# Kernel optimization log

Hardware: AMD Instinct MI355X
Metric: run time of the kernel (lower is better)

## Reference

```python
import jax, jax.numpy as jnp
import numpy as np

INPUT_DIM = 128
HIDDEN_DIM = 128
N_PATIENTS = 200000
N_CONDITIONS = 5000
N_EDGES = 1000000
IN_FEAT = INPUT_DIM * 2 + 1  # 257


def _linear_params(key, fan_in, fan_out):
    # torch nn.Linear default init: U(-1/sqrt(fan_in), 1/sqrt(fan_in))
    kw, kb = jax.random.split(key)
    bound = 1.0 / np.sqrt(fan_in)
    W = jax.random.uniform(kw, (fan_in, fan_out), jnp.float32, -bound, bound)
    b = jax.random.uniform(kb, (fan_out,), jnp.float32, -bound, bound)
    return W, b


def setup_inputs() -> dict:
    key = jax.random.key(0)
    ks = jax.random.split(key, 8)
    patient_embeds = jax.random.normal(ks[0], (N_PATIENTS, INPUT_DIM), jnp.float32)
    condition_embeds = jax.random.normal(ks[1], (N_CONDITIONS, INPUT_DIM), jnp.float32)
    src_idx = jax.random.randint(ks[2], (N_EDGES,), 0, N_PATIENTS)
    dst_idx = jax.random.randint(ks[3], (N_EDGES,), 0, N_CONDITIONS)
    edge_index = jnp.stack([src_idx, dst_idx], axis=0)
    tte = jax.random.uniform(ks[4], (N_EDGES,), jnp.float32)
    W1, b1 = _linear_params(ks[5], IN_FEAT, HIDDEN_DIM)
    W2, b2 = _linear_params(ks[6], HIDDEN_DIM, HIDDEN_DIM)
    k7, k8 = jax.random.split(ks[7])
    Wo, bo = _linear_params(k7, HIDDEN_DIM, 1)
    Wr, br = _linear_params(k8, IN_FEAT, HIDDEN_DIM)
    return {
        "patient_embeds": patient_embeds,
        "condition_embeds": condition_embeds,
        "edge_index": edge_index,
        "tte": tte,
        "W1": W1, "b1": b1,
        "W2": W2, "b2": b2,
        "Wo": Wo, "bo": bo,
        "Wr": Wr, "br": br,
    }


def reference(patient_embeds, condition_embeds, edge_index, tte,
              W1, b1, W2, b2, Wo, bo, Wr, br):
    src = patient_embeds[edge_index[0]]        # [E, D]
    dst = condition_embeds[edge_index[1]]      # [E, D]
    x = jnp.concatenate([src, dst, tte[:, None]], axis=1)  # [E, 2D+1]
    h1 = jax.nn.relu(x @ W1 + b1)              # [E, H]
    res = x @ Wr + br                          # [E, H]
    h2 = jax.nn.relu(h1 @ W2 + b2 + res)       # [E, H]
    return (h2 @ Wo + bo).reshape(-1)          # [E]
```

## Files before the change

kernel.cpp:

```cpp
#include <hip/hip_runtime.h>
#include <hip/hip_bf16.h>

using u16   = unsigned short;
using u16x4 = __attribute__((ext_vector_type(4))) unsigned short;
using u16x8 = __attribute__((ext_vector_type(8))) unsigned short;
using s16x8 = __attribute__((ext_vector_type(8))) short;
using f32x4 = __attribute__((ext_vector_type(4))) float;

#define KPAD 136
#define XP   136
#define OP   264
#define EB   64

#define BARRIER() asm volatile("s_waitcnt lgkmcnt(0)\n\ts_barrier" ::: "memory")

__device__ __forceinline__ float bf2f(u16 u){
  unsigned int x = ((unsigned int)u) << 16;
  float f; __builtin_memcpy(&f, &x, 4); return f;
}
__device__ __forceinline__ u16 f2bf(float f){
  __hip_bfloat16 h = __float2bfloat16(f);
  u16 u; __builtin_memcpy(&u, &h, 2); return u;
}
__device__ __forceinline__ f32x4 mfma16(s16x8 a, s16x8 b, f32x4 c){
  return __builtin_amdgcn_mfma_f32_16x16x32_bf16(a, b, c, 0, 0, 0);
}

__global__ __launch_bounds__(256) void prep_kernel(
    const float* __restrict__ W1, const float* __restrict__ W2,
    const float* __restrict__ Wo, const float* __restrict__ Wr,
    const float* __restrict__ b1, const float* __restrict__ b2,
    const float* __restrict__ br,
    u16* __restrict__ WF, u16* __restrict__ W2T, float* __restrict__ params)
{
  const int tid = blockIdx.x*256 + threadIdx.x;
  const int nth = gridDim.x*256;
  for (int id = tid; id < 131072; id += nth){
    const int j    = id & 7;
    const int lane = (id >> 3) & 63;
    const int pair = (id >> 9) & 1;
    const int ks   = (id >> 10) & 3;
    const int nb   = (id >> 12) & 15;
    const int h    = (id >> 16) & 1;
    const int k = ks*32 + (lane >> 4)*8 + j;
    const int n = nb*16 + (lane & 15);
    const float v = ((n < 128) ? W1 : Wr)[(h*128 + k)*128 + (n & 127)];
    const u16 hi = f2bf(v);
    WF[id] = pair ? f2bf(v - bf2f(hi)) : hi;
  }
  for (int id = tid; id < 128*128; id += nth){
    const int k = id >> 7, n = id & 127;
    W2T[n*KPAD + k] = f2bf(W2[k*128 + n]);
  }
  for (int id = tid; id < 128; id += nth){
    params[id]       = W1[256*128 + id];
    params[128 + id] = Wr[256*128 + id];
    params[256 + id] = Wo[id];
    params[384 + id]       = b1[id];
    params[384 + 128 + id] = br[id] + b2[id];
  }
}

__global__ __launch_bounds__(512, 4) void mm_kernel(
    const float* __restrict__ emb, int nrows, int ntiles,
    const u16* __restrict__ WFh, const float* __restrict__ bias,
    u16* __restrict__ outbuf)
{
  __shared__ __align__(16) char smem_raw[64*XP*2*2];
  u16* xhi = (u16*)smem_raw;
  u16* xlo = xhi + 64*XP;
  u16* sO  = (u16*)smem_raw;
  const int t = threadIdx.x;
  const int l = t & 63, w = t >> 6;
  const int lrow = l & 15, lq = l >> 4;
  s16x8 wf[2][4][2];
#pragma unroll
  for (int nbh = 0; nbh < 2; ++nbh)
#pragma unroll
    for (int ks = 0; ks < 4; ++ks){
      const int nb = w + nbh*8;
      const u16* base = WFh + (size_t)((nb*4 + ks)*2)*512 + l*8;
      wf[nbh][ks][0] = *(const s16x8*)(base);
      wf[nbh][ks][1] = *(const s16x8*)(base + 512);
    }
  float bv[2][4] = {{0.f,0.f,0.f,0.f},{0.f,0.f,0.f,0.f}};
  if (bias){
#pragma unroll
    for (int nbh = 0; nbh < 2; ++nbh)
#pragma unroll
      for (int r = 0; r < 4; ++r)
        bv[nbh][r] = bias[(w + nbh*8)*16 + lq*4 + r];
  }
  for (int tile = blockIdx.x; tile < ntiles; tile += gridDim.x){
    const int row0 = tile*64;
    BARRIER();
#pragma unroll
    for (int i = 0; i < 4; ++i){
      const int f4 = i*512 + t;
      const int r = f4 >> 5, kc = f4 & 31;
      int grow = row0 + r; if (grow >= nrows) grow = nrows - 1;
      const float4 v = *(const float4*)(emb + (size_t)grow*128 + kc*4);
      const float vv[4] = {v.x, v.y, v.z, v.w};
      u16x4 h4, l4;
#pragma unroll
      for (int q = 0; q < 4; ++q){
        const u16 hi = f2bf(vv[q]);
        h4[q] = hi;
        l4[q] = f2bf(vv[q] - bf2f(hi));
      }
      *(u16x4*)(xhi + r*XP + kc*4) = h4;
      *(u16x4*)(xlo + r*XP + kc*4) = l4;
    }
    BARRIER();
    f32x4 acc[2][4];
#pragma unroll
    for (int a = 0; a < 2; ++a)
#pragma unroll
      for (int b = 0; b < 4; ++b) acc[a][b] = (f32x4){0.f,0.f,0.f,0.f};
#pragma unroll
    for (int mb = 0; mb < 4; ++mb){
      const int mro = (mb*16 + lrow)*XP + lq*8;
#pragma unroll
      for (int ks = 0; ks < 4; ++ks){
        const s16x8 xh = *(const s16x8*)(xhi + mro + ks*32);
        const s16x8 xl = *(const s16x8*)(xlo + mro + ks*32);
#pragma unroll
        for (int nbh = 0; nbh < 2; ++nbh){
          acc[nbh][mb] = mfma16(wf[nbh][ks][0], xh, acc[nbh][mb]);
          acc[nbh][mb] = mfma16(wf[nbh][ks][1], xh, acc[nbh][mb]);
          acc[nbh][mb] = mfma16(wf[nbh][ks][0], xl, acc[nbh][mb]);
        }
      }
    }
    BARRIER();
#pragma unroll
    for (int nbh = 0; nbh < 2; ++nbh)
#pragma unroll
      for (int mb = 0; mb < 4; ++mb){
        const int m = mb*16 + lrow;
        u16x4 o;
#pragma unroll
        for (int r = 0; r < 4; ++r) o[r] = f2bf(acc[nbh][mb][r] + bv[nbh][r]);
        *(u16x4*)(sO + m*OP + (w + nbh*8)*16 + lq*4) = o;
      }
    BARRIER();
#pragma unroll
    for (int i = 0; i < 4; ++i){
      const int idx = i*512 + t;
      const int m = idx >> 5, c = idx & 31;
      const int grow = row0 + m;
      if (grow < nrows){
        const u16x8 v = *(const u16x8*)(sO + m*OP + c*8);
        *(u16x8*)(outbuf + (size_t)grow*256 + c*8) = v;
      }
    }
  }
}

__global__ __launch_bounds__(512, 4) void edge_kernel(
    const int* __restrict__ ei, const float* __restrict__ tte,
    const u16* __restrict__ PP, const u16* __restrict__ CC,
    const u16* __restrict__ W2T, const float* __restrict__ params,
    const float* __restrict__ bo_p, float* __restrict__ out, int E, int ntiles)
{
  __shared__ u16 sW2T[128*KPAD];
  __shared__ u16 sA[EB*KPAD];
  __shared__ u16 sR[EB*KPAD];
  __shared__ float sw1t[128], swrt[128], sWo[128];
  __shared__ float souts[4][EB];
  const int t = threadIdx.x;
  const int l = t & 63, w = t >> 6;
  const int lrow = l & 15, lk = l >> 4;
  const int rh = w & 1, ch = w >> 1;
  const int gid = t >> 5, gl = t & 31;
  const float bo = bo_p[0];
  {
    const u16x8* g = (const u16x8*)W2T;
    u16x8* s = (u16x8*)sW2T;
    for (int i = t; i < 128*KPAD/8; i += 512) s[i] = g[i];
  }
  if (t < 128){ sw1t[t] = params[t]; swrt[t] = params[128+t]; sWo[t] = params[256+t]; }

  int tile = blockIdx.x;
  if (tile >= ntiles) return;
  float ctt[4];
  u16x8 cpv[4], ccv[4];
  {
    int cs[4], cd[4];
#pragma unroll
    for (int i = 0; i < 4; ++i){
      int e = tile*EB + i*16 + gid; if (e >= E) e = E - 1;
      cs[i] = ei[e]; cd[i] = ei[E + e]; ctt[i] = tte[e];
    }
#pragma unroll
    for (int i = 0; i < 4; ++i){
      cpv[i] = *(const u16x8*)(PP + (size_t)cs[i]*256 + gl*8);
      ccv[i] = *(const u16x8*)(CC + (size_t)cd[i]*256 + gl*8);
    }
  }
  BARRIER();

  for (; tile < ntiles; tile += gridDim.x){
    const int ntile = tile + gridDim.x;
#pragma unroll
    for (int i = 0; i < 4; ++i){
      const int e = i*16 + gid;
      const int jj = (gl & 15)*8;
      const float tt = ctt[i];
      const float* wt = (gl < 16) ? (sw1t + jj) : (swrt + jj);
      u16x8 o;
#pragma unroll
      for (int q = 0; q < 8; ++q){
        float v = bf2f(cpv[i][q]) + bf2f(ccv[i][q]) + tt * wt[q];
        if (gl < 16) v = fmaxf(v, 0.f);
        o[q] = f2bf(v);
      }
      u16* dst = (gl < 16) ? (sA + e*KPAD + jj) : (sR + e*KPAD + jj);
      *(u16x8*)dst = o;
    }
    u16x8 npv[4], ncv[4];
    float ntt[4];
    {
      int nxs[4], nxd[4];
#pragma unroll
      for (int i = 0; i < 4; ++i){
        int e = ntile*EB + i*16 + gid; if (e >= E) e = E - 1;
        nxs[i] = ei[e]; nxd[i] = ei[E + e]; ntt[i] = tte[e];
      }
#pragma unroll
      for (int i = 0; i < 4; ++i){
        npv[i] = *(const u16x8*)(PP + (size_t)nxs[i]*256 + gl*8);
        ncv[i] = *(const u16x8*)(CC + (size_t)nxd[i]*256 + gl*8);
      }
    }
    BARRIER();
    f32x4 acc[2][2];
#pragma unroll
    for (int a = 0; a < 2; ++a)
#pragma unroll
      for (int b = 0; b < 2; ++b) acc[a][b] = (f32x4){0.f,0.f,0.f,0.f};
#pragma unroll
    for (int ks = 0; ks < 4; ++ks){
      const int koff = ks*32 + lk*8;
      const s16x8 h0 = *(const s16x8*)(sA + (rh*32 + lrow)*KPAD + koff);
      const s16x8 h1 = *(const s16x8*)(sA + (rh*32 + 16 + lrow)*KPAD + koff);
      const s16x8 b0 = *(const s16x8*)(sW2T + (ch*32 + lrow)*KPAD + koff);
      const s16x8 b1 = *(const s16x8*)(sW2T + (ch*32 + 16 + lrow)*KPAD + koff);
      acc[0][0] = mfma16(b0, h0, acc[0][0]);
      acc[0][1] = mfma16(b0, h1, acc[0][1]);
      acc[1][0] = mfma16(b1, h0, acc[1][0]);
      acc[1][1] = mfma16(b1, h1, acc[1][1]);
    }
    float p[2] = {0.f, 0.f};
    float wo[2][4];
#pragma unroll
    for (int nb = 0; nb < 2; ++nb){
#pragma unroll
      for (int r = 0; r < 4; ++r) wo[nb][r] = sWo[ch*32 + nb*16 + lk*4 + r];
    }
#pragma unroll
    for (int mb = 0; mb < 2; ++mb){
      const int edge = rh*32 + mb*16 + lrow;
#pragma unroll
      for (int nb = 0; nb < 2; ++nb){
        const int col0 = ch*32 + nb*16 + lk*4;
        const u16x4 rv = *(const u16x4*)(sR + edge*KPAD + col0);
#pragma unroll
        for (int r = 0; r < 4; ++r){
          float h2 = acc[nb][mb][r] + bf2f(rv[r]);
          h2 = fmaxf(h2, 0.f);
          p[mb] += h2 * wo[nb][r];
        }
      }
      p[mb] += __shfl_xor(p[mb], 16, 64);
      p[mb] += __shfl_xor(p[mb], 32, 64);
    }
    if (lk == 0){
      souts[ch][rh*32 + lrow]      = p[0];
      souts[ch][rh*32 + 16 + lrow] = p[1];
    }
    BARRIER();
    if (t < EB){
      const int eo = tile*EB + t;
      if (eo < E)
        out[eo] = souts[0][t] + souts[1][t] + souts[2][t] + souts[3][t] + bo;
    }
    BARRIER();
#pragma unroll
    for (int i = 0; i < 4; ++i){
      ctt[i] = ntt[i]; cpv[i] = npv[i]; ccv[i] = ncv[i];
    }
  }
}

__global__ __launch_bounds__(256) void fallback_kernel(
    const float* __restrict__ pe, const float* __restrict__ ce,
    const int* __restrict__ ei, const float* __restrict__ tte,
    const float* __restrict__ W1, const float* __restrict__ b1,
    const float* __restrict__ W2, const float* __restrict__ b2,
    const float* __restrict__ Wo, const float* __restrict__ bo,
    const float* __restrict__ Wr, const float* __restrict__ br,
    float* __restrict__ out, int E)
{
  __shared__ float sh1[4][128];
  const int w = threadIdx.x >> 6, l = threadIdx.x & 63;
  const int e_raw = blockIdx.x*4 + w;
  const int e = e_raw < E ? e_raw : E-1;
  const int s = ei[e], d = ei[E + e];
  const float tt = tte[e];
  const float* xs = pe + (size_t)s*128;
  const float* xd = ce + (size_t)d*128;
  const float x0 = xs[l], x1 = xs[64+l], x2 = xd[l], x3 = xd[64+l];
  float h1a = b1[l], h1b = b1[64+l];
  float ra = br[l], rb = br[64+l];
  for (int k = 0; k < 256; ++k){
    const float xv = (k < 64) ? x0 : (k < 128) ? x1 : (k < 192) ? x2 : x3;
    const float xk = __shfl(xv, k & 63, 64);
    h1a += xk * W1[k*128 + l];
    h1b += xk * W1[k*128 + 64 + l];
    ra  += xk * Wr[k*128 + l];
    rb  += xk * Wr[k*128 + 64 + l];
  }
  h1a += tt * W1[256*128 + l];  h1b += tt * W1[256*128 + 64 + l];
  ra  += tt * Wr[256*128 + l];  rb  += tt * Wr[256*128 + 64 + l];
  sh1[w][l] = fmaxf(h1a, 0.f);
  sh1[w][64+l] = fmaxf(h1b, 0.f);
  __syncthreads();
  float h2a = b2[l] + ra, h2b = b2[64+l] + rb;
  for (int k = 0; k < 128; ++k){
    const float hk = sh1[w][k];
    h2a += hk * W2[k*128 + l];
    h2b += hk * W2[k*128 + 64 + l];
  }
  float sum = fmaxf(h2a,0.f)*Wo[l] + fmaxf(h2b,0.f)*Wo[64+l];
  for (int off = 1; off < 64; off <<= 1) sum += __shfl_xor(sum, off, 64);
  if (l == 0 && e_raw < E) out[e_raw] = sum + bo[0];
}

extern "C" void kernel_launch(void* const* d_in, const int* in_sizes, int n_in,
                              void* d_out, int out_size, void* d_ws, size_t ws_size,
                              hipStream_t stream)
{
  const float* pe  = (const float*)d_in[0];
  const float* ce  = (const float*)d_in[1];
  const int*   ei  = (const int*)d_in[2];
  const float* tte = (const float*)d_in[3];
  const float* W1  = (const float*)d_in[4];
  const float* b1  = (const float*)d_in[5];
  const float* W2  = (const float*)d_in[6];
  const float* b2  = (const float*)d_in[7];
  const float* Wo  = (const float*)d_in[8];
  const float* bo  = (const float*)d_in[9];
  const float* Wr  = (const float*)d_in[10];
  const float* br  = (const float*)d_in[11];
  float* out = (float*)d_out;
  const int E = in_sizes[3];
  const int npat  = in_sizes[0] / 128;
  const int ncond = in_sizes[1] / 128;

  char* ws = (char*)d_ws;
  const size_t sz_PP  = (size_t)npat  * 256 * 2;
  const size_t sz_CC  = (size_t)ncond * 256 * 2;
  const size_t sz_WF  = (size_t)131072 * 2;
  const size_t sz_W2T = (size_t)128 * KPAD * 2;
  const size_t off_PP  = 0;
  const size_t off_CC  = off_PP + sz_PP;
  const size_t off_WF  = off_CC + sz_CC;
  const size_t off_W2T = off_WF + sz_WF;
  const size_t off_params = off_W2T + sz_W2T;
  const size_t ws_needed = off_params + 640*4;

  if (ws_size >= ws_needed){
    u16* PP     = (u16*)(ws + off_PP);
    u16* CCb    = (u16*)(ws + off_CC);
    u16* WF     = (u16*)(ws + off_WF);
    u16* W2T    = (u16*)(ws + off_W2T);
    float* params = (float*)(ws + off_params);
    prep_kernel<<<64, 256, 0, stream>>>(W1, W2, Wo, Wr, b1, b2, br, WF, W2T, params);
    const int ptiles = (npat + 63)/64;
    mm_kernel<<<(ptiles < 512 ? ptiles : 512), 512, 0, stream>>>(pe, npat, ptiles, WF, nullptr, PP);
    const int ctiles = (ncond + 63)/64;
    mm_kernel<<<(ctiles < 512 ? ctiles : 512), 512, 0, stream>>>(ce, ncond, ctiles, WF + 65536, params + 384, CCb);
    const int etiles = (E + EB - 1)/EB;
    edge_kernel<<<(etiles < 512 ? etiles : 512), 512, 0, stream>>>(ei, tte, PP, CCb, W2T, params, bo, out, E, etiles);
  } else {
    fallback_kernel<<<(E + 3)/4, 256, 0, stream>>>(pe, ce, ei, tte, W1, b1, W2, b2, Wo, bo, Wr, br, out, E);
  }
}
```

Measured before the change: 326.3 us.

## Stream weight fragments per k-step in mm_kernel and deepen edge gather pipeline

mm_kernel no longer keeps all weight fragments in registers. Each k-step reloads them from global memory, and each wave now owns two adjacent column blocks. This frees registers so the kernel can run at 6 blocks per SM, and the grid grows to 768. The global loads for a tile are batched before conversion, and edge_kernel prefetches edge indices two tiles ahead, issues the row gathers earlier, drops a barrier and raises wave priority around the MFMA loop. The cost is repeated weight reads per tile and a removed barrier that must remain safe.

```diff
diff --git a/kernel.cpp b/kernel.cpp
--- a/kernel.cpp
+++ b/kernel.cpp
@@ -61,9 +61,10 @@
   }
 }
 
-__global__ __launch_bounds__(512, 4) void mm_kernel(
+__global__ __launch_bounds__(512, 6) void mm_kernel(
     const float* __restrict__ emb, int nrows, int ntiles,
-    const u16* __restrict__ WFh, const float* __restrict__ bias,
+    const u16* __restrict__ WFh,
+    const float* __restrict__ bias,
     u16* __restrict__ outbuf)
 {
   __shared__ __align__(16) char smem_raw[64*XP*2*2];
@@ -73,43 +74,34 @@
   const int t = threadIdx.x;
   const int l = t & 63, w = t >> 6;
   const int lrow = l & 15, lq = l >> 4;
-  s16x8 wf[2][4][2];
-#pragma unroll
-  for (int nbh = 0; nbh < 2; ++nbh)
-#pragma unroll
-    for (int ks = 0; ks < 4; ++ks){
-      const int nb = w + nbh*8;
-      const u16* base = WFh + (size_t)((nb*4 + ks)*2)*512 + l*8;
-      wf[nbh][ks][0] = *(const s16x8*)(base);
-      wf[nbh][ks][1] = *(const s16x8*)(base + 512);
-    }
-  float bv[2][4] = {{0.f,0.f,0.f,0.f},{0.f,0.f,0.f,0.f}};
-  if (bias){
-#pragma unroll
-    for (int nbh = 0; nbh < 2; ++nbh)
-#pragma unroll
-      for (int r = 0; r < 4; ++r)
-        bv[nbh][r] = bias[(w + nbh*8)*16 + lq*4 + r];
-  }
+
   for (int tile = blockIdx.x; tile < ntiles; tile += gridDim.x){
     const int row0 = tile*64;
     BARRIER();
-#pragma unroll
-    for (int i = 0; i < 4; ++i){
-      const int f4 = i*512 + t;
-      const int r = f4 >> 5, kc = f4 & 31;
-      int grow = row0 + r; if (grow >= nrows) grow = nrows - 1;
-      const float4 v = *(const float4*)(emb + (size_t)grow*128 + kc*4);
-      const float vv[4] = {v.x, v.y, v.z, v.w};
-      u16x4 h4, l4;
-#pragma unroll
-      for (int q = 0; q < 4; ++q){
-        const u16 hi = f2bf(vv[q]);
-        h4[q] = hi;
-        l4[q] = f2bf(vv[q] - bf2f(hi));
-      }
-      *(u16x4*)(xhi + r*XP + kc*4) = h4;
-      *(u16x4*)(xlo + r*XP + kc*4) = l4;
+    {
+      float4 v[4];
+#pragma unroll
+      for (int i = 0; i < 4; ++i){
+        const int f4 = i*512 + t;
+        const int r = f4 >> 5;
+        int grow = row0 + r; if (grow >= nrows) grow = nrows - 1;
+        v[i] = *(const float4*)(emb + (size_t)grow*128 + (f4 & 31)*4);
+      }
+#pragma unroll
+      for (int i = 0; i < 4; ++i){
+        const int f4 = i*512 + t;
+        const int r = f4 >> 5, kc = f4 & 31;
+        const float vv[4] = {v[i].x, v[i].y, v[i].z, v[i].w};
+        u16x4 h4, l4;
+#pragma unroll
+        for (int q = 0; q < 4; ++q){
+          const u16 hi = f2bf(vv[q]);
+          h4[q] = hi;
+          l4[q] = f2bf(vv[q] - bf2f(hi));
+        }
+        *(u16x4*)(xhi + r*XP + kc*4) = h4;
+        *(u16x4*)(xlo + r*XP + kc*4) = l4;
+      }
     }
     BARRIER();
     f32x4 acc[2][4];
@@ -118,31 +110,42 @@
 #pragma unroll
       for (int b = 0; b < 4; ++b) acc[a][b] = (f32x4){0.f,0.f,0.f,0.f};
 #pragma unroll
-    for (int mb = 0; mb < 4; ++mb){
-      const int mro = (mb*16 + lrow)*XP + lq*8;
-#pragma unroll
-      for (int ks = 0; ks < 4; ++ks){
-        const s16x8 xh = *(const s16x8*)(xhi + mro + ks*32);
-        const s16x8 xl = *(const s16x8*)(xlo + mro + ks*32);
-#pragma unroll
-        for (int nbh = 0; nbh < 2; ++nbh){
-          acc[nbh][mb] = mfma16(wf[nbh][ks][0], xh, acc[nbh][mb]);
-          acc[nbh][mb] = mfma16(wf[nbh][ks][1], xh, acc[nbh][mb]);
-          acc[nbh][mb] = mfma16(wf[nbh][ks][0], xl, acc[nbh][mb]);
-        }
-      }
-    }
-    BARRIER();
-#pragma unroll
-    for (int nbh = 0; nbh < 2; ++nbh)
+    for (int ks = 0; ks < 4; ++ks){
+      const u16* fb = WFh + (size_t)(((2*w)*4 + ks)*2)*512 + l*8;
+      const s16x8 wh0 = *(const s16x8*)(fb);
+      const s16x8 wl0 = *(const s16x8*)(fb + 512);
+      const s16x8 wh1 = *(const s16x8*)(fb + 4096);
+      const s16x8 wl1 = *(const s16x8*)(fb + 4608);
+#pragma unroll
+      for (int mb = 0; mb < 4; ++mb){
+        const int mro = (mb*16 + lrow)*XP + lq*8 + ks*32;
+        const s16x8 xh = *(const s16x8*)(xhi + mro);
+        const s16x8 xl = *(const s16x8*)(xlo + mro);
+        acc[0][mb] = mfma16(wh0, xh, acc[0][mb]);
+        acc[0][mb] = mfma16(wl0, xh, acc[0][mb]);
+        acc[0][mb] = mfma16(wh0, xl, acc[0][mb]);
+        acc[1][mb] = mfma16(wh1, xh, acc[1][mb]);
+        acc[1][mb] = mfma16(wl1, xh, acc[1][mb]);
+        acc[1][mb] = mfma16(wh1, xl, acc[1][mb]);
+      }
+    }
+    BARRIER();
+#pragma unroll
+    for (int nb = 0; nb < 2; ++nb){
+      float bb[4] = {0.f,0.f,0.f,0.f};
+      if (bias){
+        const float4 b4 = *(const float4*)(bias + w*32 + nb*16 + lq*4);
+        bb[0] = b4.x; bb[1] = b4.y; bb[2] = b4.z; bb[3] = b4.w;
+      }
 #pragma unroll
       for (int mb = 0; mb < 4; ++mb){
         const int m = mb*16 + lrow;
         u16x4 o;
 #pragma unroll
-        for (int r = 0; r < 4; ++r) o[r] = f2bf(acc[nbh][mb][r] + bv[nbh][r]);
-        *(u16x4*)(sO + m*OP + (w + nbh*8)*16 + lq*4) = o;
-      }
+        for (int r = 0; r < 4; ++r) o[r] = f2bf(acc[nb][mb][r] + bb[r]);
+        *(u16x4*)(sO + m*OP + w*32 + nb*16 + lq*4) = o;
+      }
+    }
     BARRIER();
 #pragma unroll
     for (int i = 0; i < 4; ++i){
@@ -183,8 +186,10 @@
 
   int tile = blockIdx.x;
   if (tile >= ntiles) return;
+  const int g1 = gridDim.x;
   float ctt[4];
   u16x8 cpv[4], ccv[4];
+  int ns[4], nd[4]; float ntt[4];
   {
     int cs[4], cd[4];
 #pragma unroll
@@ -197,11 +202,21 @@
       cpv[i] = *(const u16x8*)(PP + (size_t)cs[i]*256 + gl*8);
       ccv[i] = *(const u16x8*)(CC + (size_t)cd[i]*256 + gl*8);
     }
+#pragma unroll
+    for (int i = 0; i < 4; ++i){
+      int e = (tile + g1)*EB + i*16 + gid; if (e >= E) e = E - 1;
+      ns[i] = ei[e]; nd[i] = ei[E + e]; ntt[i] = tte[e];
+    }
   }
   BARRIER();
 
-  for (; tile < ntiles; tile += gridDim.x){
-    const int ntile = tile + gridDim.x;
+  for (; tile < ntiles; tile += g1){
+    u16x8 npv[4], ncv[4];
+#pragma unroll
+    for (int i = 0; i < 4; ++i){
+      npv[i] = *(const u16x8*)(PP + (size_t)ns[i]*256 + gl*8);
+      ncv[i] = *(const u16x8*)(CC + (size_t)nd[i]*256 + gl*8);
+    }
 #pragma unroll
     for (int i = 0; i < 4; ++i){
       const int e = i*16 + gid;
@@ -218,20 +233,12 @@
       u16* dst = (gl < 16) ? (sA + e*KPAD + jj) : (sR + e*KPAD + jj);
       *(u16x8*)dst = o;
     }
-    u16x8 npv[4], ncv[4];
-    float ntt[4];
-    {
-      int nxs[4], nxd[4];
-#pragma unroll
-      for (int i = 0; i < 4; ++i){
-        int e = ntile*EB + i*16 + gid; if (e >= E) e = E - 1;
-        nxs[i] = ei[e]; nxd[i] = ei[E + e]; ntt[i] = tte[e];
-      }
-#pragma unroll
-      for (int i = 0; i < 4; ++i){
-        npv[i] = *(const u16x8*)(PP + (size_t)nxs[i]*256 + gl*8);
-        ncv[i] = *(const u16x8*)(CC + (size_t)nxd[i]*256 + gl*8);
-      }
+#pragma unroll
+    for (int i = 0; i < 4; ++i) ctt[i] = ntt[i];
+#pragma unroll
+    for (int i = 0; i < 4; ++i){
+      int e = (tile + 2*g1)*EB + i*16 + gid; if (e >= E) e = E - 1;
+      ns[i] = ei[e]; nd[i] = ei[E + e]; ntt[i] = tte[e];
     }
     BARRIER();
     f32x4 acc[2][2];
@@ -239,6 +246,7 @@
     for (int a = 0; a < 2; ++a)
 #pragma unroll
       for (int b = 0; b < 2; ++b) acc[a][b] = (f32x4){0.f,0.f,0.f,0.f};
+    __builtin_amdgcn_s_setprio(1);
 #pragma unroll
     for (int ks = 0; ks < 4; ++ks){
       const int koff = ks*32 + lk*8;
@@ -251,6 +259,7 @@
       acc[1][0] = mfma16(b1, h0, acc[1][0]);
       acc[1][1] = mfma16(b1, h1, acc[1][1]);
     }
+    __builtin_amdgcn_s_setprio(0);
     float p[2] = {0.f, 0.f};
     float wo[2][4];
 #pragma unroll
@@ -285,11 +294,8 @@
       if (eo < E)
         out[eo] = souts[0][t] + souts[1][t] + souts[2][t] + souts[3][t] + bo;
     }
-    BARRIER();
-#pragma unroll
-    for (int i = 0; i < 4; ++i){
-      ctt[i] = ntt[i]; cpv[i] = npv[i]; ccv[i] = ncv[i];
-    }
+#pragma unroll
+    for (int i = 0; i < 4; ++i){ cpv[i] = npv[i]; ccv[i] = ncv[i]; }
   }
 }
 
@@ -378,9 +384,9 @@
     float* params = (float*)(ws + off_params);
     prep_kernel<<<64, 256, 0, stream>>>(W1, W2, Wo, Wr, b1, b2, br, WF, W2T, params);
     const int ptiles = (npat + 63)/64;
-    mm_kernel<<<(ptiles < 512 ? ptiles : 512), 512, 0, stream>>>(pe, npat, ptiles, WF, nullptr, PP);
+    mm_kernel<<<(ptiles < 768 ? ptiles : 768), 512, 0, stream>>>(pe, npat, ptiles, WF, nullptr, PP);
     const int ctiles = (ncond + 63)/64;
-    mm_kernel<<<(ctiles < 512 ? ctiles : 512), 512, 0, stream>>>(ce, ncond, ctiles, WF + 65536, params + 384, CCb);
+    mm_kernel<<<(ctiles < 768 ? ctiles : 768), 512, 0, stream>>>(ce, ncond, ctiles, WF + 65536, params + 384, CCb);
     const int etiles = (E + EB - 1)/EB;
     edge_kernel<<<(etiles < 512 ? etiles : 512), 512, 0, stream>>>(ei, tte, PP, CCb, W2T, params, bo, out, E, etiles);
   } else {
```

Result: slower. 369.7 us (+13.3%).
